# Kernel tuning notes

Measured on AMD Instinct MI355X. Metric: run time of the kernel, lower is better.

Reference implementation:

```python
import jax, jax.numpy as jnp
import numpy as np

D = 1024   # dim_mid
H = 16     # heads
DK = D // H  # d_k = d_v = 64
S = 2048   # seq_len
B = 1      # batch (module's reshape logic assumes batch==1)
EPS = 1e-5


def setup_inputs() -> dict:
    key = jax.random.key(0)
    ks = jax.random.split(key, 10)
    s = 0.02
    return dict(
        Q=jax.random.normal(ks[0], (B, S, D), dtype=jnp.float32),
        K=jax.random.normal(ks[1], (B, S, D), dtype=jnp.float32),
        V=jax.random.normal(ks[2], (B, S, D), dtype=jnp.float32),
        attn_mask=jax.random.randint(ks[3], (1, S, S), 0, 2).astype(bool),
        wq=jax.random.normal(ks[4], (H * DK, D), dtype=jnp.float32) * s,
        bq=jnp.zeros((H * DK,), dtype=jnp.float32),
        wk=jax.random.normal(ks[5], (H * DK, D), dtype=jnp.float32) * s,
        bk=jnp.zeros((H * DK,), dtype=jnp.float32),
        wv=jax.random.normal(ks[6], (H * DK, D), dtype=jnp.float32) * s,
        bv=jnp.zeros((H * DK,), dtype=jnp.float32),
        wo=jax.random.normal(ks[7], (D, H * DK), dtype=jnp.float32) * s,
        bo=jnp.zeros((D,), dtype=jnp.float32),
        gamma=jnp.ones((D,), dtype=jnp.float32),
        beta=jnp.zeros((D,), dtype=jnp.float32),
    )


def reference(Q, K, V, attn_mask, wq, bq, wk, bk, wv, bv, wo, bo, gamma, beta):
    b, s = Q.shape[0], Q.shape[1]
    # projections -> (B, H, S, d_k)
    q = (Q @ wq.T + bq).reshape(b, s, H, DK).transpose(0, 2, 1, 3)
    k = (K @ wk.T + bk).reshape(b, s, H, DK).transpose(0, 2, 1, 3)
    v = (V @ wv.T + bv).reshape(b, s, H, DK).transpose(0, 2, 1, 3)
    scores = jnp.einsum('bhqd,bhkd->bhqk', q, k) / np.float32(np.sqrt(DK))
    scores = jnp.where(attn_mask[:, None, :, :], jnp.float32(-1e9), scores)
    attn = jax.nn.softmax(scores, axis=-1)
    ctx = jnp.einsum('bhqk,bhkd->bhqd', attn, v)  # (B, H, S, d_v)
    # torch: squeeze(0).transpose(0,1).view(seq_len, -1, H*d_v)  (valid for B==1)
    ctx2 = ctx[0].transpose(1, 0, 2).reshape(s, 1, H * DK)  # (S, 1, H*d_v)
    out = (ctx2 @ wo.T + bo).transpose(1, 0, 2) + Q  # (1, S, D) residual
    mu = out.mean(-1, keepdims=True)
    var = out.var(-1, keepdims=True)
    out = (out - mu) / jnp.sqrt(var + EPS) * gamma + beta
    return out, attn, ctx2
```

## Files before the change

### kernel.cpp

```cpp
#include <hip/hip_runtime.h>
#include <stdint.h>

#define S_LEN 2048
#define D_MID 1024
#define N_HEADS 16
#define D_HEAD 64

typedef __attribute__((ext_vector_type(4))) float f32x4;
typedef __attribute__((ext_vector_type(8))) short bf16x8;

__device__ __forceinline__ unsigned short f2bf(float x) {
  unsigned int u = __builtin_bit_cast(unsigned int, x);
  u += 0x7fffu + ((u >> 16) & 1u);
  return (unsigned short)(u >> 16);
}
__device__ __forceinline__ float bf2f(unsigned short h) {
  unsigned int u = ((unsigned int)h) << 16;
  return __builtin_bit_cast(float, u);
}
__device__ __forceinline__ unsigned int pack2(float x, float y) {
  return (unsigned int)f2bf(x) | ((unsigned int)f2bf(y) << 16);
}
__device__ __forceinline__ bf16x8 pack8(f32x4 a, f32x4 b) {
  uint4 u;
  u.x = pack2(a.x, a.y); u.y = pack2(a.z, a.w);
  u.z = pack2(b.x, b.y); u.w = pack2(b.z, b.w);
  return __builtin_bit_cast(bf16x8, u);
}

#define MFMA16(a, b, c) __builtin_amdgcn_mfma_f32_16x16x32_bf16((a), (b), (c), 0, 0, 0)

struct ProjParams {
  const float* A[3];
  const float* W[3];
  const float* B[3];
  unsigned short* O[3];
};

__global__ __launch_bounds__(256) void gemm_proj(ProjParams P) {
  const int z = blockIdx.z;
  const float* __restrict__ A = P.A[z];
  const float* __restrict__ W = P.W[z];
  const float* __restrict__ bias = P.B[z];
  unsigned short* __restrict__ O = P.O[z];

  __shared__ __align__(16) unsigned short As[128][56];
  __shared__ __align__(16) unsigned short Bs[128][56];

  const int tid = threadIdx.x;
  const int lane = tid & 63, w = tid >> 6;
  const int wm = w >> 1, wn = w & 1;
  const int l15 = lane & 15, lhi = lane >> 4;
  const int m0 = blockIdx.y * 128, n0 = blockIdx.x * 128;
  const int sr = tid >> 1, sc = (tid & 1) * 16;

  f32x4 acc[4][4] = {};

  for (int k0 = 0; k0 < D_MID; k0 += 32) {
    __syncthreads();
    {
      const float* a = A + (size_t)(m0 + sr) * D_MID + k0 + sc;
      float4 a0 = ((const float4*)a)[0], a1 = ((const float4*)a)[1];
      float4 a2 = ((const float4*)a)[2], a3 = ((const float4*)a)[3];
      uint4 wa0, wa1;
      wa0.x = pack2(a0.x, a0.y); wa0.y = pack2(a0.z, a0.w);
      wa0.z = pack2(a1.x, a1.y); wa0.w = pack2(a1.z, a1.w);
      wa1.x = pack2(a2.x, a2.y); wa1.y = pack2(a2.z, a2.w);
      wa1.z = pack2(a3.x, a3.y); wa1.w = pack2(a3.z, a3.w);
      *(uint4*)&As[sr][sc] = wa0;
      *(uint4*)&As[sr][sc + 8] = wa1;

      const float* b = W + (size_t)(n0 + sr) * D_MID + k0 + sc;
      float4 b0 = ((const float4*)b)[0], b1 = ((const float4*)b)[1];
      float4 b2 = ((const float4*)b)[2], b3 = ((const float4*)b)[3];
      uint4 wb0, wb1;
      wb0.x = pack2(b0.x, b0.y); wb0.y = pack2(b0.z, b0.w);
      wb0.z = pack2(b1.x, b1.y); wb0.w = pack2(b1.z, b1.w);
      wb1.x = pack2(b2.x, b2.y); wb1.y = pack2(b2.z, b2.w);
      wb1.z = pack2(b3.x, b3.y); wb1.w = pack2(b3.z, b3.w);
      *(uint4*)&Bs[sr][sc] = wb0;
      *(uint4*)&Bs[sr][sc + 8] = wb1;
    }
    __syncthreads();

    bf16x8 af[4], bfr[4];
#pragma unroll
    for (int a = 0; a < 4; ++a)
      af[a] = *(const bf16x8*)&As[wm * 64 + a * 16 + l15][lhi * 8];
#pragma unroll
    for (int b = 0; b < 4; ++b)
      bfr[b] = *(const bf16x8*)&Bs[wn * 64 + b * 16 + l15][lhi * 8];
#pragma unroll
    for (int a = 0; a < 4; ++a)
#pragma unroll
      for (int b = 0; b < 4; ++b) acc[a][b] = MFMA16(af[a], bfr[b], acc[a][b]);
  }

#pragma unroll
  for (int a = 0; a < 4; ++a)
#pragma unroll
    for (int b = 0; b < 4; ++b) {
      const int col = n0 + wn * 64 + b * 16 + l15;
      const float bv = bias[col];
#pragma unroll
      for (int j = 0; j < 4; ++j) {
        const int row = m0 + wm * 64 + a * 16 + lhi * 4 + j;
        O[(size_t)row * D_MID + col] = f2bf(acc[a][b][j] + bv);
      }
    }
}

__global__ __launch_bounds__(256) void gemm_out(
    const float* __restrict__ Actx, const float* __restrict__ W,
    const float* __restrict__ bias, const float* __restrict__ resid,
    float* __restrict__ Of) {
  __shared__ __align__(16) unsigned short As[128][56];
  __shared__ __align__(16) unsigned short Bs[128][56];

  const int tid = threadIdx.x;
  const int lane = tid & 63, w = tid >> 6;
  const int wm = w >> 1, wn = w & 1;
  const int l15 = lane & 15, lhi = lane >> 4;
  const int m0 = blockIdx.y * 128, n0 = blockIdx.x * 128;
  const int sr = tid >> 1, sc = (tid & 1) * 16;

  f32x4 acc[4][4] = {};

  for (int k0 = 0; k0 < D_MID; k0 += 32) {
    __syncthreads();
    {
      const float* a = Actx + (size_t)(m0 + sr) * D_MID + k0 + sc;
      float4 a0 = ((const float4*)a)[0], a1 = ((const float4*)a)[1];
      float4 a2 = ((const float4*)a)[2], a3 = ((const float4*)a)[3];
      uint4 wa0, wa1;
      wa0.x = pack2(a0.x, a0.y); wa0.y = pack2(a0.z, a0.w);
      wa0.z = pack2(a1.x, a1.y); wa0.w = pack2(a1.z, a1.w);
      wa1.x = pack2(a2.x, a2.y); wa1.y = pack2(a2.z, a2.w);
      wa1.z = pack2(a3.x, a3.y); wa1.w = pack2(a3.z, a3.w);
      *(uint4*)&As[sr][sc] = wa0;
      *(uint4*)&As[sr][sc + 8] = wa1;

      const float* b = W + (size_t)(n0 + sr) * D_MID + k0 + sc;
      float4 b0 = ((const float4*)b)[0], b1 = ((const float4*)b)[1];
      float4 b2 = ((const float4*)b)[2], b3 = ((const float4*)b)[3];
      uint4 wb0, wb1;
      wb0.x = pack2(b0.x, b0.y); wb0.y = pack2(b0.z, b0.w);
      wb0.z = pack2(b1.x, b1.y); wb0.w = pack2(b1.z, b1.w);
      wb1.x = pack2(b2.x, b2.y); wb1.y = pack2(b2.z, b2.w);
      wb1.z = pack2(b3.x, b3.y); wb1.w = pack2(b3.z, b3.w);
      *(uint4*)&Bs[sr][sc] = wb0;
      *(uint4*)&Bs[sr][sc + 8] = wb1;
    }
    __syncthreads();

    bf16x8 af[4], bfr[4];
#pragma unroll
    for (int a = 0; a < 4; ++a)
      af[a] = *(const bf16x8*)&As[wm * 64 + a * 16 + l15][lhi * 8];
#pragma unroll
    for (int b = 0; b < 4; ++b)
      bfr[b] = *(const bf16x8*)&Bs[wn * 64 + b * 16 + l15][lhi * 8];
#pragma unroll
    for (int a = 0; a < 4; ++a)
#pragma unroll
      for (int b = 0; b < 4; ++b) acc[a][b] = MFMA16(af[a], bfr[b], acc[a][b]);
  }

#pragma unroll
  for (int a = 0; a < 4; ++a)
#pragma unroll
    for (int b = 0; b < 4; ++b) {
      const int col = n0 + wn * 64 + b * 16 + l15;
      const float bv = bias[col];
#pragma unroll
      for (int j = 0; j < 4; ++j) {
        const int row = m0 + wm * 64 + a * 16 + lhi * 4 + j;
        Of[(size_t)row * D_MID + col] =
            acc[a][b][j] + bv + resid[(size_t)row * D_MID + col];
      }
    }
}

__global__ __launch_bounds__(256) void transpose_to_vbt(
    const unsigned short* __restrict__ v, unsigned short* __restrict__ vt) {
  __shared__ __align__(16) unsigned short t[64][72];
  const int tid = threadIdx.x;
  const int bs = blockIdx.x * 64;
  const int bd = blockIdx.y * 64;
  {
    const int r = tid >> 2, c = (tid & 3) * 16;
    const unsigned short* src = v + (size_t)(bs + r) * D_MID + bd + c;
    *(uint4*)&t[r][c] = *(const uint4*)src;
    *(uint4*)&t[r][c + 8] = *(const uint4*)(src + 8);
  }
  __syncthreads();
  {
    const int d = tid >> 2, c = (tid & 3) * 16;
    unsigned int u[8];
#pragma unroll
    for (int jj = 0; jj < 8; ++jj)
      u[jj] = (unsigned int)t[c + 2 * jj][d] | ((unsigned int)t[c + 2 * jj + 1][d] << 16);
    uint4 w0, w1;
    w0.x = u[0]; w0.y = u[1]; w0.z = u[2]; w0.w = u[3];
    w1.x = u[4]; w1.y = u[5]; w1.z = u[6]; w1.w = u[7];
    unsigned short* dst = vt + (size_t)(bd + d) * S_LEN + bs + c;
    *(uint4*)dst = w0;
    *(uint4*)(dst + 8) = w1;
  }
}

__global__ __launch_bounds__(256) void pack_mask(const void* __restrict__ maskp,
                                                 unsigned long long* __restrict__ bits) {
  __shared__ int s_m32;
  if (threadIdx.x == 0) s_m32 = 1;
  __syncthreads();
  {
    const unsigned char* m8d = (const unsigned char*)maskp;
    bool nz = false;
    for (int i = threadIdx.x; i < 4096; i += 256)
      if (i & 3) nz |= (m8d[i] != 0);
    if (nz) s_m32 = 0;
  }
  __syncthreads();

  const int wi = blockIdx.x * 256 + threadIdx.x;
  const int row = wi >> 5, chunk = wi & 31;
  unsigned long long keep = 0ull;
  if (s_m32) {
    const int* mi = (const int*)maskp + (size_t)row * S_LEN + chunk * 64;
#pragma unroll
    for (int q = 0; q < 16; ++q) {
      int4 v = ((const int4*)mi)[q];
      const int b = q * 4;
      if (!v.x) keep |= 1ull << b;
      if (!v.y) keep |= 1ull << (b + 1);
      if (!v.z) keep |= 1ull << (b + 2);
      if (!v.w) keep |= 1ull << (b + 3);
    }
  } else {
    const unsigned char* p = (const unsigned char*)maskp + (size_t)row * S_LEN + chunk * 64;
    union { uint4 v[4]; unsigned char c[64]; } u;
#pragma unroll
    for (int q = 0; q < 4; ++q) u.v[q] = ((const uint4*)p)[q];
#pragma unroll
    for (int b = 0; b < 64; ++b)
      if (!u.c[b]) keep |= 1ull << b;
  }
  bits[wi] = keep;
}

__global__ __launch_bounds__(256) void lsum_kernel(
    const unsigned short* __restrict__ qb, const unsigned short* __restrict__ kb,
    const unsigned long long* __restrict__ bits, float* __restrict__ lpart) {
  const int bid = blockIdx.x;
  const int head = bid & 15;
  const int r = bid >> 4;
  const int q0 = (r & 31) * 64;
  const int kc = r >> 5;
  const int k0 = kc * (S_LEN / 4);

  const int tid = threadIdx.x;
  const int lane = tid & 63, w = tid >> 6;
  const int l15 = lane & 15, lhi = lane >> 4;

  __shared__ __align__(16) unsigned short Kt[64][72];

  bf16x8 aq[2];
  {
    const unsigned short* qp =
        qb + (size_t)(q0 + w * 16 + l15) * D_MID + head * D_HEAD + lhi * 8;
    aq[0] = *(const bf16x8*)qp;
    aq[1] = *(const bf16x8*)(qp + 32);
  }

  float plrow[4] = {0.f, 0.f, 0.f, 0.f};
  const int sk = tid >> 2, sc = (tid & 3) * 16;

  const int ntiles = (S_LEN / 4) / 64;
  uint4 kr0, kr1;
  {
    const unsigned short* src = kb + (size_t)(k0 + sk) * D_MID + head * D_HEAD + sc;
    kr0 = *(const uint4*)src;
    kr1 = *(const uint4*)(src + 8);
  }

  for (int t = 0; t < ntiles; ++t) {
    const int kt = k0 + t * 64;
    __syncthreads();
    *(uint4*)&Kt[sk][sc] = kr0;
    *(uint4*)&Kt[sk][sc + 8] = kr1;
    __syncthreads();
    if (t + 1 < ntiles) {
      const unsigned short* src =
          kb + (size_t)(kt + 64 + sk) * D_MID + head * D_HEAD + sc;
      kr0 = *(const uint4*)src;
      kr1 = *(const uint4*)(src + 8);
    }

    f32x4 sacc[4];
#pragma unroll
    for (int a = 0; a < 4; ++a) {
      bf16x8 b0 = *(const bf16x8*)&Kt[a * 16 + l15][lhi * 8];
      bf16x8 b1 = *(const bf16x8*)&Kt[a * 16 + l15][32 + lhi * 8];
      f32x4 t2 = {0.f, 0.f, 0.f, 0.f};
      t2 = MFMA16(aq[0], b0, t2);
      t2 = MFMA16(aq[1], b1, t2);
      sacc[a] = t2;
    }

#pragma unroll
    for (int j = 0; j < 4; ++j) {
      const int qg = q0 + w * 16 + lhi * 4 + j;
      const unsigned long long w64 = bits[(size_t)qg * 32 + (kt >> 6)];
#pragma unroll
      for (int a = 0; a < 4; ++a) {
        const float keep = (float)((w64 >> (a * 16 + l15)) & 1ull);
        plrow[j] += __expf(sacc[a][j] * 0.125f) * keep;
      }
    }
  }

#pragma unroll
  for (int j = 0; j < 4; ++j) {
    float ts = plrow[j];
#pragma unroll
    for (int off = 1; off < 16; off <<= 1) ts += __shfl_xor(ts, off);
    plrow[j] = ts;
  }
  if (l15 == 0) {
#pragma unroll
    for (int j = 0; j < 4; ++j) {
      const int qg = q0 + w * 16 + lhi * 4 + j;
      lpart[((size_t)kc * N_HEADS + head) * S_LEN + qg] = plrow[j];
    }
  }
}

__global__ __launch_bounds__(256) void lcombine(const float* __restrict__ lpart,
                                                float* __restrict__ linv) {
  const int i = blockIdx.x * 256 + threadIdx.x;
  const float s = lpart[i] + lpart[32768 + i] + lpart[65536 + i] + lpart[98304 + i];
  linv[i] = (s > 0.f) ? 1.f / s : 0.f;
}

__global__ __launch_bounds__(256) void attn_main(
    const unsigned short* __restrict__ qb, const unsigned short* __restrict__ kb,
    const unsigned short* __restrict__ vbt, const unsigned long long* __restrict__ bits,
    const float* __restrict__ linv, float* __restrict__ attn_out,
    unsigned short* __restrict__ ctxp, int nkc) {
  const int bid = blockIdx.x;
  const int head = bid & 15;
  const int r = bid >> 4;
  const int q0 = (r & 31) * 64;
  const int kc = r >> 5;
  const int kspan = S_LEN / nkc;
  const int k_begin = kc * kspan;

  const int tid = threadIdx.x;
  const int lane = tid & 63, w = tid >> 6;
  const int l15 = lane & 15, lhi = lane >> 4;

  __shared__ __align__(16) unsigned short Kt[64][72];
  __shared__ __align__(16) unsigned short Vt[64][72];
  __shared__ __align__(16) float PF[4][16][68];

  bf16x8 aq[2];
  float li[4];
  {
    const int qrow = q0 + w * 16 + l15;
    const unsigned short* qp = qb + (size_t)qrow * D_MID + head * D_HEAD + lhi * 8;
    aq[0] = *(const bf16x8*)qp;
    aq[1] = *(const bf16x8*)(qp + 32);
#pragma unroll
    for (int j = 0; j < 4; ++j)
      li[j] = linv[head * S_LEN + q0 + w * 16 + lhi * 4 + j];
  }

  f32x4 cacc[4] = {};
  const int sk = tid >> 2, sc = (tid & 3) * 16;
  const int ntiles = kspan / 64;

  uint4 kr0, kr1, vr0, vr1;
  {
    const unsigned short* srck = kb + (size_t)(k_begin + sk) * D_MID + head * D_HEAD + sc;
    kr0 = *(const uint4*)srck;
    kr1 = *(const uint4*)(srck + 8);
    const unsigned short* srcv = vbt + (size_t)(head * D_HEAD + sk) * S_LEN + k_begin + sc;
    vr0 = *(const uint4*)srcv;
    vr1 = *(const uint4*)(srcv + 8);
  }

  for (int t = 0; t < ntiles; ++t) {
    const int kt = k_begin + t * 64;
    __syncthreads();
    *(uint4*)&Kt[sk][sc] = kr0;
    *(uint4*)&Kt[sk][sc + 8] = kr1;
    *(uint4*)&Vt[sk][sc] = vr0;
    *(uint4*)&Vt[sk][sc + 8] = vr1;
    __syncthreads();
    if (t + 1 < ntiles) {
      const int kn = kt + 64;
      const unsigned short* srck = kb + (size_t)(kn + sk) * D_MID + head * D_HEAD + sc;
      kr0 = *(const uint4*)srck;
      kr1 = *(const uint4*)(srck + 8);
      const unsigned short* srcv = vbt + (size_t)(head * D_HEAD + sk) * S_LEN + kn + sc;
      vr0 = *(const uint4*)srcv;
      vr1 = *(const uint4*)(srcv + 8);
    }

    f32x4 sacc[4];
#pragma unroll
    for (int a = 0; a < 4; ++a) {
      bf16x8 b0 = *(const bf16x8*)&Kt[a * 16 + l15][lhi * 8];
      bf16x8 b1 = *(const bf16x8*)&Kt[a * 16 + l15][32 + lhi * 8];
      f32x4 t2 = {0.f, 0.f, 0.f, 0.f};
      t2 = MFMA16(aq[0], b0, t2);
      t2 = MFMA16(aq[1], b1, t2);
      sacc[a] = t2;
    }

#pragma unroll
    for (int j = 0; j < 4; ++j) {
      const int qg = q0 + w * 16 + lhi * 4 + j;
      const unsigned long long w64 = bits[(size_t)qg * 32 + (kt >> 6)];
#pragma unroll
      for (int a = 0; a < 4; ++a) {
        const float keep = (float)((w64 >> (a * 16 + l15)) & 1ull);
        PF[w][lhi * 4 + j][a * 16 + l15] = __expf(sacc[a][j] * 0.125f) * keep * li[j];
      }
    }

    {
      float* abase = attn_out + (size_t)head * S_LEN * S_LEN +
                     (size_t)(q0 + w * 16) * S_LEN + kt;
#pragma unroll
      for (int g = 0; g < 4; ++g) {
        const int row = g * 4 + lhi;
        f32x4 v = *(const f32x4*)&PF[w][row][l15 * 4];
        __builtin_nontemporal_store(v, (f32x4*)(abase + (size_t)row * S_LEN + l15 * 4));
      }
    }

    bf16x8 pa0 = pack8(*(const f32x4*)&PF[w][l15][lhi * 8],
                       *(const f32x4*)&PF[w][l15][lhi * 8 + 4]);
    bf16x8 pa1 = pack8(*(const f32x4*)&PF[w][l15][32 + lhi * 8],
                       *(const f32x4*)&PF[w][l15][36 + lhi * 8]);
#pragma unroll
    for (int n = 0; n < 4; ++n) {
      bf16x8 v0 = *(const bf16x8*)&Vt[n * 16 + l15][lhi * 8];
      bf16x8 v1 = *(const bf16x8*)&Vt[n * 16 + l15][32 + lhi * 8];
      cacc[n] = MFMA16(pa0, v0, cacc[n]);
      cacc[n] = MFMA16(pa1, v1, cacc[n]);
    }
  }

  unsigned short* cp = ctxp + (size_t)kc * S_LEN * D_MID;
#pragma unroll
  for (int n = 0; n < 4; ++n)
#pragma unroll
    for (int j = 0; j < 4; ++j) {
      const int qg = q0 + w * 16 + lhi * 4 + j;
      const int col = head * D_HEAD + n * 16 + l15;
      cp[(size_t)qg * D_MID + col] = f2bf(cacc[n][j]);
    }
}

__global__ __launch_bounds__(256) void ctx_reduce(const unsigned short* __restrict__ ctxp,
                                                  float* __restrict__ ctx2, int nkc) {
  const int i = blockIdx.x * 256 + threadIdx.x;
  ushort4 a = ((const ushort4*)ctxp)[i];
  float4 o;
  o.x = bf2f(a.x); o.y = bf2f(a.y); o.z = bf2f(a.z); o.w = bf2f(a.w);
  if (nkc == 2) {
    ushort4 b = ((const ushort4*)(ctxp + (size_t)S_LEN * D_MID))[i];
    o.x += bf2f(b.x); o.y += bf2f(b.y); o.z += bf2f(b.z); o.w += bf2f(b.w);
  }
  ((float4*)ctx2)[i] = o;
}

__global__ __launch_bounds__(256) void layernorm_k(
    const float* __restrict__ x, const float* __restrict__ gamma,
    const float* __restrict__ beta, float* __restrict__ out) {
  const int row = blockIdx.x;
  const int tid = threadIdx.x;
  float4 v = ((const float4*)(x + (size_t)row * D_MID))[tid];
  float s = v.x + v.y + v.z + v.w;
  float s2 = v.x * v.x + v.y * v.y + v.z * v.z + v.w * v.w;
#pragma unroll
  for (int off = 1; off < 64; off <<= 1) {
    s += __shfl_xor(s, off);
    s2 += __shfl_xor(s2, off);
  }
  __shared__ float ps[4], ps2[4];
  const int w = tid >> 6;
  if ((tid & 63) == 0) { ps[w] = s; ps2[w] = s2; }
  __syncthreads();
  s = ps[0] + ps[1] + ps[2] + ps[3];
  s2 = ps2[0] + ps2[1] + ps2[2] + ps2[3];
  const float mu = s * (1.0f / D_MID);
  const float var = s2 * (1.0f / D_MID) - mu * mu;
  const float inv = rsqrtf(var + 1e-5f);
  float4 g = ((const float4*)gamma)[tid];
  float4 b = ((const float4*)beta)[tid];
  float4 o;
  o.x = (v.x - mu) * inv * g.x + b.x;
  o.y = (v.y - mu) * inv * g.y + b.y;
  o.z = (v.z - mu) * inv * g.z + b.z;
  o.w = (v.w - mu) * inv * g.w + b.w;
  ((float4*)(out + (size_t)row * D_MID))[tid] = o;
}

extern "C" void kernel_launch(void* const* d_in, const int* in_sizes, int n_in,
                              void* d_out, int out_size, void* d_ws, size_t ws_size,
                              hipStream_t stream) {
  (void)in_sizes; (void)n_in; (void)out_size;
  const float* Q = (const float*)d_in[0];
  const float* K = (const float*)d_in[1];
  const float* V = (const float*)d_in[2];
  const void* mask = d_in[3];
  const float* wq = (const float*)d_in[4];
  const float* bq = (const float*)d_in[5];
  const float* wk = (const float*)d_in[6];
  const float* bk = (const float*)d_in[7];
  const float* wv = (const float*)d_in[8];
  const float* bv = (const float*)d_in[9];
  const float* wo = (const float*)d_in[10];
  const float* bo = (const float*)d_in[11];
  const float* gamma = (const float*)d_in[12];
  const float* beta = (const float*)d_in[13];

  float* out = (float*)d_out;
  float* attn = out + (size_t)S_LEN * D_MID;
  float* ctx2 = attn + (size_t)N_HEADS * S_LEN * S_LEN;

  unsigned char* ws = (unsigned char*)d_ws;
  unsigned short* qb   = (unsigned short*)(ws);
  unsigned short* kbuf = (unsigned short*)(ws + (size_t)(4 << 20));
  unsigned short* vbuf = (unsigned short*)(ws + (size_t)(8 << 20));
  unsigned short* vbt  = (unsigned short*)(ws + (size_t)(12 << 20));
  unsigned long long* bits = (unsigned long long*)(ws + (size_t)(16 << 20));
  float* lpart = (float*)(ws + (size_t)(16 << 20) + 524288);
  float* linv  = (float*)(ws + (size_t)(17 << 20) + 262144);
  unsigned short* ctxp = (unsigned short*)(ws + (size_t)(18 << 20));
  float* preLN = (float*)(ws);

  const size_t need2 = (size_t)(18 << 20) + 2 * (size_t)S_LEN * D_MID * 2;
  const int nkc = (ws_size >= need2) ? 2 : 1;

  ProjParams pp;
  pp.A[0] = Q;  pp.W[0] = wq; pp.B[0] = bq; pp.O[0] = qb;
  pp.A[1] = K;  pp.W[1] = wk; pp.B[1] = bk; pp.O[1] = kbuf;
  pp.A[2] = V;  pp.W[2] = wv; pp.B[2] = bv; pp.O[2] = vbuf;

  gemm_proj<<<dim3(D_MID / 128, S_LEN / 128, 3), 256, 0, stream>>>(pp);
  pack_mask<<<256, 256, 0, stream>>>(mask, bits);
  transpose_to_vbt<<<dim3(S_LEN / 64, D_MID / 64), 256, 0, stream>>>(vbuf, vbt);
  lsum_kernel<<<2048, 256, 0, stream>>>(qb, kbuf, bits, lpart);
  lcombine<<<128, 256, 0, stream>>>(lpart, linv);
  attn_main<<<512 * nkc, 256, 0, stream>>>(qb, kbuf, vbt, bits, linv, attn, ctxp, nkc);
  ctx_reduce<<<(S_LEN * D_MID / 4) / 256, 256, 0, stream>>>(ctxp, ctx2, nkc);
  gemm_out<<<dim3(D_MID / 128, S_LEN / 128), 256, 0, stream>>>(ctx2, wo, bo, Q, preLN);
  layernorm_k<<<S_LEN, 256, 0, stream>>>(preLN, gamma, beta, out);
}
```

Measured before the change: 230.8 us.

## Pre-convert weights to bf16 and double GEMM K-tile with hardware pack

```diff
diff --git a/kernel.cpp b/kernel.cpp
--- a/kernel.cpp
+++ b/kernel.cpp
@@ -27,156 +27,167 @@
   u.z = pack2(b.x, b.y); u.w = pack2(b.z, b.w);
   return __builtin_bit_cast(bf16x8, u);
 }
+__device__ __forceinline__ unsigned int cvtpk(float lo, float hi) {
+  unsigned int r;
+  asm("v_cvt_pk_bf16_f32 %0, %1, %2" : "=v"(r) : "v"(lo), "v"(hi));
+  return r;
+}
 
 #define MFMA16(a, b, c) __builtin_amdgcn_mfma_f32_16x16x32_bf16((a), (b), (c), 0, 0, 0)
+
+struct CvtP {
+  const float* s[4];
+  unsigned short* d[4];
+};
+__global__ __launch_bounds__(256) void cvt_w(CvtP P) {
+  const int t = blockIdx.x * 256 + threadIdx.x;
+  const int seg = t >> 17;
+  const int off = (t & 131071) * 8;
+  const float* s = P.s[seg] + off;
+  f32x4 x = *(const f32x4*)s, y = *(const f32x4*)(s + 4);
+  uint4 u;
+  u.x = cvtpk(x.x, x.y); u.y = cvtpk(x.z, x.w);
+  u.z = cvtpk(y.x, y.y); u.w = cvtpk(y.z, y.w);
+  *(uint4*)(P.d[seg] + off) = u;
+}
 
 struct ProjParams {
   const float* A[3];
-  const float* W[3];
-  const float* B[3];
+  const unsigned short* W[3];
+  const float* Bi[3];
   unsigned short* O[3];
 };
 
 __global__ __launch_bounds__(256) void gemm_proj(ProjParams P) {
   const int z = blockIdx.z;
   const float* __restrict__ A = P.A[z];
-  const float* __restrict__ W = P.W[z];
-  const float* __restrict__ bias = P.B[z];
+  const unsigned short* __restrict__ W = P.W[z];
+  const float* __restrict__ bias = P.Bi[z];
   unsigned short* __restrict__ O = P.O[z];
 
-  __shared__ __align__(16) unsigned short As[128][56];
-  __shared__ __align__(16) unsigned short Bs[128][56];
+  __shared__ __align__(16) unsigned short As[128][72];
+  __shared__ __align__(16) unsigned short Bs[128][72];
 
   const int tid = threadIdx.x;
   const int lane = tid & 63, w = tid >> 6;
   const int wm = w >> 1, wn = w & 1;
   const int l15 = lane & 15, lhi = lane >> 4;
   const int m0 = blockIdx.y * 128, n0 = blockIdx.x * 128;
-  const int sr = tid >> 1, sc = (tid & 1) * 16;
+  const int sr = tid >> 1, sc = (tid & 1) * 32;
 
   f32x4 acc[4][4] = {};
 
-  for (int k0 = 0; k0 < D_MID; k0 += 32) {
+  for (int k0 = 0; k0 < D_MID; k0 += 64) {
     __syncthreads();
     {
       const float* a = A + (size_t)(m0 + sr) * D_MID + k0 + sc;
-      float4 a0 = ((const float4*)a)[0], a1 = ((const float4*)a)[1];
-      float4 a2 = ((const float4*)a)[2], a3 = ((const float4*)a)[3];
-      uint4 wa0, wa1;
-      wa0.x = pack2(a0.x, a0.y); wa0.y = pack2(a0.z, a0.w);
-      wa0.z = pack2(a1.x, a1.y); wa0.w = pack2(a1.z, a1.w);
-      wa1.x = pack2(a2.x, a2.y); wa1.y = pack2(a2.z, a2.w);
-      wa1.z = pack2(a3.x, a3.y); wa1.w = pack2(a3.z, a3.w);
-      *(uint4*)&As[sr][sc] = wa0;
-      *(uint4*)&As[sr][sc + 8] = wa1;
-
-      const float* b = W + (size_t)(n0 + sr) * D_MID + k0 + sc;
-      float4 b0 = ((const float4*)b)[0], b1 = ((const float4*)b)[1];
-      float4 b2 = ((const float4*)b)[2], b3 = ((const float4*)b)[3];
-      uint4 wb0, wb1;
-      wb0.x = pack2(b0.x, b0.y); wb0.y = pack2(b0.z, b0.w);
-      wb0.z = pack2(b1.x, b1.y); wb0.w = pack2(b1.z, b1.w);
-      wb1.x = pack2(b2.x, b2.y); wb1.y = pack2(b2.z, b2.w);
-      wb1.z = pack2(b3.x, b3.y); wb1.w = pack2(b3.z, b3.w);
-      *(uint4*)&Bs[sr][sc] = wb0;
-      *(uint4*)&Bs[sr][sc + 8] = wb1;
-    }
-    __syncthreads();
-
-    bf16x8 af[4], bfr[4];
-#pragma unroll
-    for (int a = 0; a < 4; ++a)
-      af[a] = *(const bf16x8*)&As[wm * 64 + a * 16 + l15][lhi * 8];
-#pragma unroll
-    for (int b = 0; b < 4; ++b)
-      bfr[b] = *(const bf16x8*)&Bs[wn * 64 + b * 16 + l15][lhi * 8];
-#pragma unroll
-    for (int a = 0; a < 4; ++a)
-#pragma unroll
-      for (int b = 0; b < 4; ++b) acc[a][b] = MFMA16(af[a], bfr[b], acc[a][b]);
-  }
-
-#pragma unroll
-  for (int a = 0; a < 4; ++a)
-#pragma unroll
-    for (int b = 0; b < 4; ++b) {
-      const int col = n0 + wn * 64 + b * 16 + l15;
+      const unsigned short* b = W + (size_t)(n0 + sr) * D_MID + k0 + sc;
+#pragma unroll
+      for (int q = 0; q < 4; ++q) {
+        f32x4 x = ((const f32x4*)a)[2 * q];
+        f32x4 y = ((const f32x4*)a)[2 * q + 1];
+        uint4 u;
+        u.x = cvtpk(x.x, x.y); u.y = cvtpk(x.z, x.w);
+        u.z = cvtpk(y.x, y.y); u.w = cvtpk(y.z, y.w);
+        *(uint4*)&As[sr][sc + q * 8] = u;
+        *(uint4*)&Bs[sr][sc + q * 8] = ((const uint4*)b)[q];
+      }
+    }
+    __syncthreads();
+
+    bf16x8 af[4][2], bfr[4][2];
+#pragma unroll
+    for (int a2 = 0; a2 < 4; ++a2) {
+      af[a2][0] = *(const bf16x8*)&As[wm * 64 + a2 * 16 + l15][lhi * 8];
+      af[a2][1] = *(const bf16x8*)&As[wm * 64 + a2 * 16 + l15][32 + lhi * 8];
+      bfr[a2][0] = *(const bf16x8*)&Bs[wn * 64 + a2 * 16 + l15][lhi * 8];
+      bfr[a2][1] = *(const bf16x8*)&Bs[wn * 64 + a2 * 16 + l15][32 + lhi * 8];
+    }
+#pragma unroll
+    for (int a2 = 0; a2 < 4; ++a2)
+#pragma unroll
+      for (int b2 = 0; b2 < 4; ++b2) {
+        acc[a2][b2] = MFMA16(af[a2][0], bfr[b2][0], acc[a2][b2]);
+        acc[a2][b2] = MFMA16(af[a2][1], bfr[b2][1], acc[a2][b2]);
+      }
+  }
+
+#pragma unroll
+  for (int a2 = 0; a2 < 4; ++a2)
+#pragma unroll
+    for (int b2 = 0; b2 < 4; ++b2) {
+      const int col = n0 + wn * 64 + b2 * 16 + l15;
       const float bv = bias[col];
 #pragma unroll
       for (int j = 0; j < 4; ++j) {
-        const int row = m0 + wm * 64 + a * 16 + lhi * 4 + j;
-        O[(size_t)row * D_MID + col] = f2bf(acc[a][b][j] + bv);
+        const int row = m0 + wm * 64 + a2 * 16 + lhi * 4 + j;
+        O[(size_t)row * D_MID + col] = f2bf(acc[a2][b2][j] + bv);
       }
     }
 }
 
 __global__ __launch_bounds__(256) void gemm_out(
-    const float* __restrict__ Actx, const float* __restrict__ W,
+    const float* __restrict__ Actx, const unsigned short* __restrict__ W,
     const float* __restrict__ bias, const float* __restrict__ resid,
     float* __restrict__ Of) {
-  __shared__ __align__(16) unsigned short As[128][56];
-  __shared__ __align__(16) unsigned short Bs[128][56];
+  __shared__ __align__(16) unsigned short As[128][72];
+  __shared__ __align__(16) unsigned short Bs[128][72];
 
   const int tid = threadIdx.x;
   const int lane = tid & 63, w = tid >> 6;
   const int wm = w >> 1, wn = w & 1;
   const int l15 = lane & 15, lhi = lane >> 4;
   const int m0 = blockIdx.y * 128, n0 = blockIdx.x * 128;
-  const int sr = tid >> 1, sc = (tid & 1) * 16;
+  const int sr = tid >> 1, sc = (tid & 1) * 32;
 
   f32x4 acc[4][4] = {};
 
-  for (int k0 = 0; k0 < D_MID; k0 += 32) {
+  for (int k0 = 0; k0 < D_MID; k0 += 64) {
     __syncthreads();
     {
       const float* a = Actx + (size_t)(m0 + sr) * D_MID + k0 + sc;
-      float4 a0 = ((const float4*)a)[0], a1 = ((const float4*)a)[1];
-      float4 a2 = ((const float4*)a)[2], a3 = ((const float4*)a)[3];
-      uint4 wa0, wa1;
-      wa0.x = pack2(a0.x, a0.y); wa0.y = pack2(a0.z, a0.w);
-      wa0.z = pack2(a1.x, a1.y); wa0.w = pack2(a1.z, a1.w);
-      wa1.x = pack2(a2.x, a2.y); wa1.y = pack2(a2.z, a2.w);
-      wa1.z = pack2(a3.x, a3.y); wa1.w = pack2(a3.z, a3.w);
-      *(uint4*)&As[sr][sc] = wa0;
-      *(uint4*)&As[sr][sc + 8] = wa1;
-
-      const float* b = W + (size_t)(n0 + sr) * D_MID + k0 + sc;
-      float4 b0 = ((const float4*)b)[0], b1 = ((const float4*)b)[1];
-      float4 b2 = ((const float4*)b)[2], b3 = ((const float4*)b)[3];
-      uint4 wb0, wb1;
-      wb0.x = pack2(b0.x, b0.y); wb0.y = pack2(b0.z, b0.w);
-      wb0.z = pack2(b1.x, b1.y); wb0.w = pack2(b1.z, b1.w);
-      wb1.x = pack2(b2.x, b2.y); wb1.y = pack2(b2.z, b2.w);
-      wb1.z = pack2(b3.x, b3.y); wb1.w = pack2(b3.z, b3.w);
-      *(uint4*)&Bs[sr][sc] = wb0;
-      *(uint4*)&Bs[sr][sc + 8] = wb1;
-    }
-    __syncthreads();
-
-    bf16x8 af[4], bfr[4];
-#pragma unroll
-    for (int a = 0; a < 4; ++a)
-      af[a] = *(const bf16x8*)&As[wm * 64 + a * 16 + l15][lhi * 8];
-#pragma unroll
-    for (int b = 0; b < 4; ++b)
-      bfr[b] = *(const bf16x8*)&Bs[wn * 64 + b * 16 + l15][lhi * 8];
-#pragma unroll
-    for (int a = 0; a < 4; ++a)
-#pragma unroll
-      for (int b = 0; b < 4; ++b) acc[a][b] = MFMA16(af[a], bfr[b], acc[a][b]);
-  }
-
-#pragma unroll
-  for (int a = 0; a < 4; ++a)
-#pragma unroll
-    for (int b = 0; b < 4; ++b) {
-      const int col = n0 + wn * 64 + b * 16 + l15;
+      const unsigned short* b = W + (size_t)(n0 + sr) * D_MID + k0 + sc;
+#pragma unroll
+      for (int q = 0; q < 4; ++q) {
+        f32x4 x = ((const f32x4*)a)[2 * q];
+        f32x4 y = ((const f32x4*)a)[2 * q + 1];
+        uint4 u;
+        u.x = cvtpk(x.x, x.y); u.y = cvtpk(x.z, x.w);
+        u.z = cvtpk(y.x, y.y); u.w = cvtpk(y.z, y.w);
+        *(uint4*)&As[sr][sc + q * 8] = u;
+        *(uint4*)&Bs[sr][sc + q * 8] = ((const uint4*)b)[q];
+      }
+    }
+    __syncthreads();
+
+    bf16x8 af[4][2], bfr[4][2];
+#pragma unroll
+    for (int a2 = 0; a2 < 4; ++a2) {
+      af[a2][0] = *(const bf16x8*)&As[wm * 64 + a2 * 16 + l15][lhi * 8];
+      af[a2][1] = *(const bf16x8*)&As[wm * 64 + a2 * 16 + l15][32 + lhi * 8];
+      bfr[a2][0] = *(const bf16x8*)&Bs[wn * 64 + a2 * 16 + l15][lhi * 8];
+      bfr[a2][1] = *(const bf16x8*)&Bs[wn * 64 + a2 * 16 + l15][32 + lhi * 8];
+    }
+#pragma unroll
+    for (int a2 = 0; a2 < 4; ++a2)
+#pragma unroll
+      for (int b2 = 0; b2 < 4; ++b2) {
+        acc[a2][b2] = MFMA16(af[a2][0], bfr[b2][0], acc[a2][b2]);
+        acc[a2][b2] = MFMA16(af[a2][1], bfr[b2][1], acc[a2][b2]);
+      }
+  }
+
+#pragma unroll
+  for (int a2 = 0; a2 < 4; ++a2)
+#pragma unroll
+    for (int b2 = 0; b2 < 4; ++b2) {
+      const int col = n0 + wn * 64 + b2 * 16 + l15;
       const float bv = bias[col];
 #pragma unroll
       for (int j = 0; j < 4; ++j) {
-        const int row = m0 + wm * 64 + a * 16 + lhi * 4 + j;
+        const int row = m0 + wm * 64 + a2 * 16 + lhi * 4 + j;
         Of[(size_t)row * D_MID + col] =
-            acc[a][b][j] + bv + resid[(size_t)row * D_MID + col];
+            acc[a2][b2][j] + bv + resid[(size_t)row * D_MID + col];
       }
     }
 }
@@ -541,16 +552,26 @@
   unsigned long long* bits = (unsigned long long*)(ws + (size_t)(16 << 20));
   float* lpart = (float*)(ws + (size_t)(16 << 20) + 524288);
   float* linv  = (float*)(ws + (size_t)(17 << 20) + 262144);
+  unsigned short* wqb = (unsigned short*)(ws + (size_t)(18 << 20));
+  unsigned short* wkb = (unsigned short*)(ws + (size_t)(20 << 20));
+  unsigned short* wvb = (unsigned short*)(ws + (size_t)(22 << 20));
   unsigned short* ctxp = (unsigned short*)(ws + (size_t)(18 << 20));
+  unsigned short* wob = (unsigned short*)(ws + (size_t)(26 << 20));
   float* preLN = (float*)(ws);
 
-  const size_t need2 = (size_t)(18 << 20) + 2 * (size_t)S_LEN * D_MID * 2;
-  const int nkc = (ws_size >= need2) ? 2 : 1;
+  const int nkc = 2;
+
+  CvtP cw;
+  cw.s[0] = wq; cw.d[0] = wqb;
+  cw.s[1] = wk; cw.d[1] = wkb;
+  cw.s[2] = wv; cw.d[2] = wvb;
+  cw.s[3] = wo; cw.d[3] = wob;
+  cvt_w<<<2048, 256, 0, stream>>>(cw);
 
   ProjParams pp;
-  pp.A[0] = Q;  pp.W[0] = wq; pp.B[0] = bq; pp.O[0] = qb;
-  pp.A[1] = K;  pp.W[1] = wk; pp.B[1] = bk; pp.O[1] = kbuf;
-  pp.A[2] = V;  pp.W[2] = wv; pp.B[2] = bv; pp.O[2] = vbuf;
+  pp.A[0] = Q;  pp.W[0] = wqb; pp.Bi[0] = bq; pp.O[0] = qb;
+  pp.A[1] = K;  pp.W[1] = wkb; pp.Bi[1] = bk; pp.O[1] = kbuf;
+  pp.A[2] = V;  pp.W[2] = wvb; pp.Bi[2] = bv; pp.O[2] = vbuf;
 
   gemm_proj<<<dim3(D_MID / 128, S_LEN / 128, 3), 256, 0, stream>>>(pp);
   pack_mask<<<256, 256, 0, stream>>>(mask, bits);
@@ -559,6 +580,6 @@
   lcombine<<<128, 256, 0, stream>>>(lpart, linv);
   attn_main<<<512 * nkc, 256, 0, stream>>>(qb, kbuf, vbt, bits, linv, attn, ctxp, nkc);
   ctx_reduce<<<(S_LEN * D_MID / 4) / 256, 256, 0, stream>>>(ctxp, ctx2, nkc);
-  gemm_out<<<dim3(D_MID / 128, S_LEN / 128), 256, 0, stream>>>(ctx2, wo, bo, Q, preLN);
+  gemm_out<<<dim3(D_MID / 128, S_LEN / 128), 256, 0, stream>>>(ctx2, wob, bo, Q, preLN);
   layernorm_k<<<S_LEN, 256, 0, stream>>>(preLN, gamma, beta, out);
 }
```

Result: no change. 230.3 us (median of 2 runs) (-0.2%).
